# Kernel tuning notes

Measured on AMD Instinct MI355X. Metric: run time of the kernel, lower is better.

The kernel has to match this reference:

```python
import jax, jax.numpy as jnp
import numpy as np

EPS = 1e-5

def _proj(x, w, b, gamma, beta, mean, var):
    # 1x1 conv (einsum over channels) + BatchNorm (inference) ; Dropout is identity in eval.
    y = jnp.einsum('bchw,oc->bohw', x, w) + b[None, :, None, None]
    scale = gamma * jax.lax.rsqrt(var + EPS)
    shift = beta - mean * scale
    return y * scale[None, :, None, None] + shift[None, :, None, None]

def _make_layer(key, cin, cout):
    k1, k2, k3, k4 = jax.random.split(key, 4)
    w = jax.random.normal(k1, (cout, cin), jnp.float32) * (1.0 / np.sqrt(cin))
    b = jax.random.normal(k2, (cout,), jnp.float32) * 0.01
    gamma = 1.0 + 0.1 * jax.random.normal(k3, (cout,), jnp.float32)
    beta = 0.1 * jax.random.normal(k4, (cout,), jnp.float32)
    mean = 0.05 * jax.random.normal(jax.random.fold_in(k1, 7), (cout,), jnp.float32)
    var = 0.5 + jax.random.uniform(jax.random.fold_in(k2, 7), (cout,), jnp.float32)
    return w, b, gamma, beta, mean, var

def setup_inputs() -> dict:
    key = jax.random.key(0)
    B, C, Ci, H, W = 4, 128, 64, 64, 64
    ks = jax.random.split(key, 6)
    inp = {
        'x1': jax.random.normal(ks[0], (B, C, H, W), jnp.float32),
        'x2': jax.random.normal(ks[1], (B, C, H, W), jnp.float32),
    }
    for name, k, cin, cout in [('theta', ks[2], C, Ci), ('phi', ks[3], C, Ci),
                               ('g', ks[4], C, Ci), ('wout', ks[5], Ci, C)]:
        w, b, gm, bt, mn, vr = _make_layer(k, cin, cout)
        inp.update({f'{name}_w': w, f'{name}_b': b, f'{name}_g': gm,
                    f'{name}_beta': bt, f'{name}_m': mn, f'{name}_v': vr})
    return inp

def reference(x1, x2,
              theta_w, theta_b, theta_g, theta_beta, theta_m, theta_v,
              phi_w, phi_b, phi_g, phi_beta, phi_m, phi_v,
              g_w, g_b, g_g, g_beta, g_m, g_v,
              wout_w, wout_b, wout_g, wout_beta, wout_m, wout_v):
    B, C, H, W = x1.shape
    N = H * W
    theta_x1 = _proj(x1, theta_w, theta_b, theta_g, theta_beta, theta_m, theta_v).reshape(B, -1, N)  # [B,Ci,N]
    phi_x2 = _proj(x2, phi_w, phi_b, phi_g, phi_beta, phi_m, phi_v).reshape(B, -1, N)                # [B,Ci,N]
    g_x2 = _proj(x2, g_w, g_b, g_g, g_beta, g_m, g_v).reshape(B, -1, N)                              # [B,Ci,N]
    # attention_map[b, n, m] = sum_c theta[b,c,n] * phi[b,c,m]
    attn = jax.nn.softmax(jnp.einsum('bcn,bcm->bnm', theta_x1, phi_x2), axis=-1)  # [B,N,N]
    out = jnp.einsum('bnm,bcm->bcn', attn, g_x2).reshape(B, -1, H, W)             # [B,Ci,H,W]
    out = _proj(out, wout_w, wout_b, wout_g, wout_beta, wout_m, wout_v)           # [B,C,H,W]
    return jnp.concatenate((out, x1), axis=1)                                     # [B,2C,H,W]
```

## Files before the change

### kernel.cpp

```cpp
#include <hip/hip_runtime.h>
#include <stdint.h>
#include <stddef.h>

#define EPS   1e-5f
#define NB    4
#define CINCH 128
#define CI    64
#define NPIX  4096

typedef __bf16 bf16_t;
typedef bf16_t bf16x8 __attribute__((ext_vector_type(8)));
typedef float  f32x4  __attribute__((ext_vector_type(4)));

__device__ __forceinline__ f32x4 mfma16(bf16x8 a, bf16x8 b, f32x4 c) {
  return __builtin_amdgcn_mfma_f32_16x16x32_bf16(a, b, c, 0, 0, 0);
}
__device__ __forceinline__ f32x4 fzero4() {
  f32x4 z = {0.f, 0.f, 0.f, 0.f};
  return z;
}


__global__ __launch_bounds__(256) void proj_theta(
    const float* __restrict__ x1,
    const float* __restrict__ w,  const float* __restrict__ bb,
    const float* __restrict__ gm, const float* __restrict__ bt,
    const float* __restrict__ mn, const float* __restrict__ vr,
    bf16_t* __restrict__ thetaT_h, bf16_t* __restrict__ thetaT_l,
    float* __restrict__ out)
{
  __shared__ float wT[CINCH][CI];
  __shared__ float bfold[CI];
  const int tid = threadIdx.x;
  const int b   = blockIdx.y;
  const int n0  = blockIdx.x * 64;

  for (int idx = tid; idx < CI * CINCH; idx += 256) {
    const int o = idx & 63;
    const int c = idx >> 6;
    const float sc = gm[o] * rsqrtf(vr[o] + EPS);
    wT[c][o] = w[o * CINCH + c] * sc;
    if (c == 0) bfold[o] = bb[o] * sc + bt[o] - mn[o] * sc;
  }
  __syncthreads();

  const int n4 = tid & 15;
  const int og = tid >> 4;
  const float* xb = x1 + (size_t)b * CINCH * NPIX + n0 + n4 * 4;

  float acc[4][4];
#pragma unroll
  for (int j = 0; j < 4; ++j)
#pragma unroll
    for (int i = 0; i < 4; ++i) acc[j][i] = 0.f;

  for (int c0 = 0; c0 < CINCH; c0 += 4) {
    f32x4 xv[4];
#pragma unroll
    for (int cc = 0; cc < 4; ++cc)
      xv[cc] = *(const f32x4*)(xb + (size_t)(c0 + cc) * NPIX);
#pragma unroll
    for (int cc = 0; cc < 4; ++cc) {
      const f32x4 wv = *(const f32x4*)&wT[c0 + cc][og * 4];
#pragma unroll
      for (int j = 0; j < 4; ++j)
#pragma unroll
        for (int i = 0; i < 4; ++i)
          acc[j][i] += wv[j] * xv[cc][i];
    }
  }

#pragma unroll
  for (int j = 0; j < 4; ++j) {
    const int o = og * 4 + j;
    const float bias = bfold[o];
#pragma unroll
    for (int i = 0; i < 4; ++i) {
      const int n = n0 + n4 * 4 + i;
      const float v = acc[j][i] + bias;
      const bf16_t h = (bf16_t)v;
      const bf16_t l = (bf16_t)(v - (float)h);
      const size_t base = ((size_t)b * NPIX + n) * CI + o;
      thetaT_h[base] = h;
      thetaT_l[base] = l;
    }
  }

  for (int k = tid; k < CINCH * 64; k += 256) {
    const int c = k >> 6, nl = k & 63;
    out[((size_t)b * 256 + 128 + c) * NPIX + n0 + nl] =
        x1[((size_t)b * CINCH + c) * NPIX + n0 + nl];
  }
}

__global__ __launch_bounds__(256) void proj_phig(
    const float* __restrict__ x2,
    const float* __restrict__ pw,  const float* __restrict__ pb,
    const float* __restrict__ pg,  const float* __restrict__ pbt,
    const float* __restrict__ pm,  const float* __restrict__ pv,
    const float* __restrict__ gw,  const float* __restrict__ gb,
    const float* __restrict__ gg,  const float* __restrict__ gbt,
    const float* __restrict__ gmn, const float* __restrict__ gv,
    bf16_t* __restrict__ phiT_h, bf16_t* __restrict__ phiT_l,
    bf16_t* __restrict__ g_cm)
{
  __shared__ float wT[CINCH][128];
  __shared__ float bfold[128];
  const int tid = threadIdx.x;
  const int b   = blockIdx.y;
  const int n0  = blockIdx.x * 64;

  for (int idx = tid; idx < 128 * CINCH; idx += 256) {
    const int o  = idx & 127;
    const int c  = idx >> 7;
    const int oo = o & 63;
    float sc, wv_, bb_, bt_, mn_;
    if (o < 64) { sc = pg[oo] * rsqrtf(pv[oo] + EPS); wv_ = pw[oo*CINCH+c]; bb_ = pb[oo]; bt_ = pbt[oo]; mn_ = pm[oo]; }
    else        { sc = gg[oo] * rsqrtf(gv[oo] + EPS); wv_ = gw[oo*CINCH+c]; bb_ = gb[oo]; bt_ = gbt[oo]; mn_ = gmn[oo]; }
    wT[c][o] = wv_ * sc;
    if (c == 0) bfold[o] = bb_ * sc + bt_ - mn_ * sc;
  }
  __syncthreads();

  const int n4 = tid & 15;
  const int og = tid >> 4;
  const float* xb = x2 + (size_t)b * CINCH * NPIX + n0 + n4 * 4;

  float acc[8][4];
#pragma unroll
  for (int j = 0; j < 8; ++j)
#pragma unroll
    for (int i = 0; i < 4; ++i) acc[j][i] = 0.f;

  for (int c0 = 0; c0 < CINCH; c0 += 4) {
    f32x4 xv[4];
#pragma unroll
    for (int cc = 0; cc < 4; ++cc)
      xv[cc] = *(const f32x4*)(xb + (size_t)(c0 + cc) * NPIX);
#pragma unroll
    for (int cc = 0; cc < 4; ++cc) {
      const f32x4 wv0 = *(const f32x4*)&wT[c0 + cc][og * 8];
      const f32x4 wv1 = *(const f32x4*)&wT[c0 + cc][og * 8 + 4];
#pragma unroll
      for (int j = 0; j < 4; ++j)
#pragma unroll
        for (int i = 0; i < 4; ++i) {
          acc[j][i]     += wv0[j] * xv[cc][i];
          acc[j + 4][i] += wv1[j] * xv[cc][i];
        }
    }
  }

#pragma unroll
  for (int j = 0; j < 8; ++j) {
    const int o = og * 8 + j;
    const float bias = bfold[o];
#pragma unroll
    for (int i = 0; i < 4; ++i) {
      const int n = n0 + n4 * 4 + i;
      const float v = acc[j][i] + bias;
      if (o < 64) {
        const bf16_t h = (bf16_t)v;
        const bf16_t l = (bf16_t)(v - (float)h);
        const size_t rowb = ((size_t)b * NPIX + n) * 128;
        const int byte = (o * 2) ^ ((n & 7) << 4);
        *(bf16_t*)((char*)phiT_h + rowb + byte) = h;
        *(bf16_t*)((char*)phiT_l + rowb + byte) = l;
      } else {
        const int c = o - 64;
        const size_t base = ((size_t)b * CI + c) * (NPIX * 2);
        const int byte = ((n & ~63) * 2) + (((n & 63) * 2) ^ ((c & 7) << 4));
        *(bf16_t*)((char*)g_cm + base + byte) = (bf16_t)v;
      }
    }
  }
}

__global__ __launch_bounds__(256, 2) void flash_attn(
    const bf16_t* __restrict__ thetaT_h, const bf16_t* __restrict__ thetaT_l,
    const bf16_t* __restrict__ phiT_h,   const bf16_t* __restrict__ phiT_l,
    const bf16_t* __restrict__ g_cm,
    float* __restrict__ Opart, float* __restrict__ mlbuf)
{
  __shared__ __attribute__((aligned(16))) char sPhiH[64 * 128];
  __shared__ __attribute__((aligned(16))) char sPhiL[64 * 128];
  __shared__ __attribute__((aligned(16))) char sV[64 * 128];
  __shared__ __attribute__((aligned(16))) char sP[4][32 * 144];

  const int tid  = threadIdx.x;
  const int lane = tid & 63;
  const int wid  = tid >> 6;
  const int lrow = lane & 15;
  const int lhi  = lane >> 4;

  const int wg = blockIdx.x;
  const int b  = wg >> 7;
  const int qt = (wg & 127) >> 2;
  const int ks = wg & 3;
  const int q0 = qt * 128 + wid * 32;
  const int m0 = ks * 1024;

  bf16x8 qh[2][2], qlv[2][2];
  {
    const bf16_t* qbh = thetaT_h + ((size_t)b * NPIX + q0 + lrow) * CI + lhi * 8;
    const bf16_t* qbl = thetaT_l + ((size_t)b * NPIX + q0 + lrow) * CI + lhi * 8;
#pragma unroll
    for (int nt = 0; nt < 2; ++nt)
#pragma unroll
      for (int kk = 0; kk < 2; ++kk) {
        qh[nt][kk]  = *(const bf16x8*)(qbh + nt * 16 * CI + kk * 32);
        qlv[nt][kk] = *(const bf16x8*)(qbl + nt * 16 * CI + kk * 32);
      }
  }

  f32x4 oacc[2][4];
#pragma unroll
  for (int a = 0; a < 2; ++a)
#pragma unroll
    for (int c = 0; c < 4; ++c) oacc[a][c] = fzero4();

  float m_run[2] = {-1e30f, -1e30f};
  float l_run[2] = {0.f, 0.f};

  char* const Pw = sP[wid];

  for (int kb = 0; kb < 16; ++kb) {
    const int mg = m0 + kb * 64;
    __syncthreads();
    {
      const char* srcPH = (const char*)phiT_h + ((size_t)b * NPIX + mg) * 128;
      const char* srcPL = (const char*)phiT_l + ((size_t)b * NPIX + mg) * 128;
#pragma unroll
      for (int r = 0; r < 6; ++r) {
        const int chunk = r * 256 + tid;
        if (chunk < 512) {
          *(f32x4*)(sPhiH + chunk * 16) = *(const f32x4*)(srcPH + chunk * 16);
        } else if (chunk < 1024) {
          const int c2 = chunk - 512;
          *(f32x4*)(sPhiL + c2 * 16) = *(const f32x4*)(srcPL + c2 * 16);
        } else {
          const int c2  = chunk - 1024;
          const int row = c2 >> 3;
          const int col = (c2 & 7) * 16;
          *(f32x4*)(sV + row * 128 + col) =
              *(const f32x4*)((const char*)g_cm +
                              ((size_t)b * CI + row) * (NPIX * 2) + mg * 2 + col);
        }
      }
    }
    __syncthreads();

    f32x4 s[4][2];
#pragma unroll
    for (int mt = 0; mt < 4; ++mt)
#pragma unroll
      for (int nt = 0; nt < 2; ++nt) s[mt][nt] = fzero4();

#pragma unroll
    for (int mt = 0; mt < 4; ++mt) {
      const int row = mt * 16 + lrow;
      const int swz = (row & 7) << 4;
#pragma unroll
      for (int kk = 0; kk < 2; ++kk) {
        const int byte = row * 128 + ((kk * 64 + lhi * 16) ^ swz);
        const bf16x8 aH = *(const bf16x8*)(sPhiH + byte);
        const bf16x8 aL = *(const bf16x8*)(sPhiL + byte);
#pragma unroll
        for (int nt = 0; nt < 2; ++nt) {
          s[mt][nt] = mfma16(aH, qh[nt][kk],  s[mt][nt]);
          s[mt][nt] = mfma16(aH, qlv[nt][kk], s[mt][nt]);
          s[mt][nt] = mfma16(aL, qh[nt][kk],  s[mt][nt]);
        }
      }
    }

    float a2[2];
#pragma unroll
    for (int nt = 0; nt < 2; ++nt) {
      float mx = -1e30f;
#pragma unroll
      for (int mt = 0; mt < 4; ++mt)
#pragma unroll
        for (int r = 0; r < 4; ++r) mx = fmaxf(mx, s[mt][nt][r]);
      mx = fmaxf(mx, __shfl_xor(mx, 16));
      mx = fmaxf(mx, __shfl_xor(mx, 32));
      const float mnew  = fmaxf(m_run[nt], mx);
      const float alpha = __expf(m_run[nt] - mnew);
      float lsum = 0.f;
#pragma unroll
      for (int mt = 0; mt < 4; ++mt)
#pragma unroll
        for (int r = 0; r < 4; ++r) {
          const float p = __expf(s[mt][nt][r] - mnew);
          s[mt][nt][r] = p;
          lsum += p;
        }
      lsum += __shfl_xor(lsum, 16);
      lsum += __shfl_xor(lsum, 32);
      l_run[nt] = l_run[nt] * alpha + lsum;
      m_run[nt] = mnew;
      a2[nt] = alpha;
    }

#pragma unroll
    for (int qt2 = 0; qt2 < 2; ++qt2) {
#pragma unroll
      for (int r = 0; r < 4; ++r) {
        const float av = __shfl(a2[qt2], lhi * 4 + r);
#pragma unroll
        for (int ct = 0; ct < 4; ++ct) oacc[qt2][ct][r] *= av;
      }
    }

#pragma unroll
    for (int mt = 0; mt < 4; ++mt)
#pragma unroll
      for (int nt = 0; nt < 2; ++nt) {
        union { bf16_t h[4]; uint32_t u[2]; } pk;
#pragma unroll
        for (int r = 0; r < 4; ++r) pk.h[r] = (bf16_t)s[mt][nt][r];
        const int q    = nt * 16 + lrow;
        const int mloc = mt * 16 + lhi * 4;
        *(uint2*)(Pw + q * 144 + mloc * 2) = make_uint2(pk.u[0], pk.u[1]);
      }

    bf16x8 bV[2][4];
#pragma unroll
    for (int ct = 0; ct < 4; ++ct) {
      const int row = ct * 16 + lrow;
      const int swz = (row & 7) << 4;
#pragma unroll
      for (int kk = 0; kk < 2; ++kk)
        bV[kk][ct] = *(const bf16x8*)(sV + row * 128 + ((kk * 64 + lhi * 16) ^ swz));
    }
#pragma unroll
    for (int qt2 = 0; qt2 < 2; ++qt2) {
#pragma unroll
      for (int kk = 0; kk < 2; ++kk) {
        const bf16x8 pfrag =
            *(const bf16x8*)(Pw + (qt2 * 16 + lrow) * 144 + kk * 64 + lhi * 16);
#pragma unroll
        for (int ct = 0; ct < 4; ++ct)
          oacc[qt2][ct] = mfma16(pfrag, bV[kk][ct], oacc[qt2][ct]);
      }
    }
  }

#pragma unroll
  for (int qt2 = 0; qt2 < 2; ++qt2)
#pragma unroll
    for (int ct = 0; ct < 4; ++ct)
#pragma unroll
      for (int r = 0; r < 4; ++r) {
        const int q = q0 + qt2 * 16 + lhi * 4 + r;
        const int c = ct * 16 + lrow;
        Opart[(((size_t)b * NPIX + q) * 4 + ks) * 64 + c] = oacc[qt2][ct][r];
      }
  if (lhi < 2) {
    const int q = q0 + lhi * 16 + lrow;
    const size_t base = (((size_t)b * NPIX + q) * 4 + ks) * 2;
    mlbuf[base]     = m_run[lhi];
    mlbuf[base + 1] = l_run[lhi];
  }
}

__global__ __launch_bounds__(256) void merge_out(
    const float* __restrict__ Opart, const float* __restrict__ mlbuf,
    const float* __restrict__ ww,  const float* __restrict__ wb,
    const float* __restrict__ wg,  const float* __restrict__ wbt,
    const float* __restrict__ wm,  const float* __restrict__ wvv,
    float* __restrict__ out)
{
  __shared__ float wlds[128][64];
  __shared__ float bfold[128];
  const int tid = threadIdx.x;
  const int b   = blockIdx.y;
  const int n0  = blockIdx.x * 64;

  for (int idx = tid; idx < 128 * 64; idx += 256) {
    const int o = idx >> 6, c = idx & 63;
    const float sc = wg[o] * rsqrtf(wvv[o] + EPS);
    wlds[o][c] = ww[o * 64 + c] * sc;
    if (c == 0) bfold[o] = wb[o] * sc + wbt[o] - wm[o] * sc;
  }
  __syncthreads();

  const int ql = tid & 63;
  const int oh = tid >> 6;
  const int q  = n0 + ql;
  const size_t sb = ((size_t)b * NPIX + q) * 4;

  float mk[4], lk[4];
#pragma unroll
  for (int ks = 0; ks < 4; ++ks) {
    mk[ks] = mlbuf[(sb + ks) * 2];
    lk[ks] = mlbuf[(sb + ks) * 2 + 1];
  }
  const float M = fmaxf(fmaxf(mk[0], mk[1]), fmaxf(mk[2], mk[3]));
  float al[4]; float den = 0.f;
#pragma unroll
  for (int ks = 0; ks < 4; ++ks) { al[ks] = __expf(mk[ks] - M); den += al[ks] * lk[ks]; }
  const float inv = 1.f / den;
#pragma unroll
  for (int ks = 0; ks < 4; ++ks) al[ks] *= inv;

  float acc[32];
#pragma unroll
  for (int j = 0; j < 32; ++j) acc[j] = 0.f;

  for (int c0 = 0; c0 < 64; c0 += 4) {
    f32x4 mrg = {0.f, 0.f, 0.f, 0.f};
#pragma unroll
    for (int ks = 0; ks < 4; ++ks) {
      const f32x4 pv4 = *(const f32x4*)(Opart + (sb + ks) * 64 + c0);
      mrg += pv4 * al[ks];
    }
#pragma unroll
    for (int j = 0; j < 32; ++j) {
      const f32x4 wv4 = *(const f32x4*)&wlds[oh * 32 + j][c0];
      acc[j] += wv4[0] * mrg[0] + wv4[1] * mrg[1] + wv4[2] * mrg[2] + wv4[3] * mrg[3];
    }
  }

#pragma unroll
  for (int j = 0; j < 32; ++j) {
    const int o = oh * 32 + j;
    out[((size_t)b * 256 + o) * NPIX + q] = acc[j] + bfold[o];
  }
}

extern "C" void kernel_launch(void* const* d_in, const int* in_sizes, int n_in,
                              void* d_out, int out_size, void* d_ws, size_t ws_size,
                              hipStream_t stream) {
  (void)in_sizes; (void)n_in; (void)out_size; (void)ws_size;
  const float* x1  = (const float*)d_in[0];
  const float* x2  = (const float*)d_in[1];
  const float* tw  = (const float*)d_in[2];
  const float* tb  = (const float*)d_in[3];
  const float* tg  = (const float*)d_in[4];
  const float* tbt = (const float*)d_in[5];
  const float* tm  = (const float*)d_in[6];
  const float* tv  = (const float*)d_in[7];
  const float* pw  = (const float*)d_in[8];
  const float* pb  = (const float*)d_in[9];
  const float* pg  = (const float*)d_in[10];
  const float* pbt = (const float*)d_in[11];
  const float* pm  = (const float*)d_in[12];
  const float* pv  = (const float*)d_in[13];
  const float* gw  = (const float*)d_in[14];
  const float* gb  = (const float*)d_in[15];
  const float* gg  = (const float*)d_in[16];
  const float* gbt = (const float*)d_in[17];
  const float* gmn = (const float*)d_in[18];
  const float* gv  = (const float*)d_in[19];
  const float* ww  = (const float*)d_in[20];
  const float* wb  = (const float*)d_in[21];
  const float* wg  = (const float*)d_in[22];
  const float* wbt = (const float*)d_in[23];
  const float* wm  = (const float*)d_in[24];
  const float* wv  = (const float*)d_in[25];

  float* out = (float*)d_out;
  char*  ws  = (char*)d_ws;
  bf16_t* thetaT_h = (bf16_t*)(ws);
  bf16_t* thetaT_l = (bf16_t*)(ws + (size_t)(2)  * 1048576);
  bf16_t* phiT_h   = (bf16_t*)(ws + (size_t)(4)  * 1048576);
  bf16_t* phiT_l   = (bf16_t*)(ws + (size_t)(6)  * 1048576);
  bf16_t* g_cm     = (bf16_t*)(ws + (size_t)(8)  * 1048576);
  float*  Opart    = (float*) (ws + (size_t)(10) * 1048576);
  float*  mlbuf    = (float*) (ws + (size_t)(26) * 1048576);

  dim3 gp(64, 4);
  proj_theta<<<gp, 256, 0, stream>>>(x1, tw, tb, tg, tbt, tm, tv,
                                     thetaT_h, thetaT_l, out);
  proj_phig<<<gp, 256, 0, stream>>>(x2, pw, pb, pg, pbt, pm, pv,
                                    gw, gb, gg, gbt, gmn, gv,
                                    phiT_h, phiT_l, g_cm);
  flash_attn<<<512, 256, 0, stream>>>(thetaT_h, thetaT_l, phiT_h, phiT_l,
                                      g_cm, Opart, mlbuf);
  merge_out<<<gp, 256, 0, stream>>>(Opart, mlbuf, ww, wb, wg, wbt, wm, wv, out);
}
```

Measured before the change: 260.6 us.

## Double-buffer attention tiles via async global-to-LDS loads and retile projection kernels

The flash attention loop now stages phi and g tiles into a double-buffered LDS region using global_load_lds, so loading the next key block overlaps compute on the current one and one barrier per iteration is dropped. The projection kernels are split (phi and g into separate kernels) and switched to 32-pixel tiles with an LDS transpose, so outputs go out as vectorized 16-byte bf16 stores instead of scalar ones. The merge kernel is restructured to merge partials into LDS first, then run the output projection with twice as many blocks. The extra kernel launch, the added LDS use, and the more complex ordering around the async loads are the costs.

```diff
diff --git a/kernel.cpp b/kernel.cpp
--- a/kernel.cpp
+++ b/kernel.cpp
@@ -3,7 +3,6 @@
 #include <stddef.h>
 
 #define EPS   1e-5f
-#define NB    4
 #define CINCH 128
 #define CI    64
 #define NPIX  4096
@@ -12,12 +11,18 @@
 typedef bf16_t bf16x8 __attribute__((ext_vector_type(8)));
 typedef float  f32x4  __attribute__((ext_vector_type(4)));
 
+typedef __attribute__((address_space(3))) unsigned int lds_u32;
+typedef __attribute__((address_space(1))) const unsigned int glb_u32;
+
 __device__ __forceinline__ f32x4 mfma16(bf16x8 a, bf16x8 b, f32x4 c) {
   return __builtin_amdgcn_mfma_f32_16x16x32_bf16(a, b, c, 0, 0, 0);
 }
 __device__ __forceinline__ f32x4 fzero4() {
   f32x4 z = {0.f, 0.f, 0.f, 0.f};
   return z;
+}
+__device__ __forceinline__ void gload16(const void* g, void* l) {
+  __builtin_amdgcn_global_load_lds((glb_u32*)g, (lds_u32*)l, 16, 0, 0);
 }
 
 
@@ -31,148 +36,202 @@
 {
   __shared__ float wT[CINCH][CI];
   __shared__ float bfold[CI];
+  __shared__ float tileF[32][68];
+
   const int tid = threadIdx.x;
   const int b   = blockIdx.y;
-  const int n0  = blockIdx.x * 64;
+  const int n0  = blockIdx.x * 32;
 
   for (int idx = tid; idx < CI * CINCH; idx += 256) {
-    const int o = idx & 63;
-    const int c = idx >> 6;
+    const int o = idx & 63, c = idx >> 6;
     const float sc = gm[o] * rsqrtf(vr[o] + EPS);
     wT[c][o] = w[o * CINCH + c] * sc;
     if (c == 0) bfold[o] = bb[o] * sc + bt[o] - mn[o] * sc;
   }
   __syncthreads();
 
-  const int n4 = tid & 15;
-  const int og = tid >> 4;
-  const float* xb = x1 + (size_t)b * CINCH * NPIX + n0 + n4 * 4;
-
-  float acc[4][4];
-#pragma unroll
-  for (int j = 0; j < 4; ++j)
-#pragma unroll
-    for (int i = 0; i < 4; ++i) acc[j][i] = 0.f;
-
+  const int px = tid & 31;
+  const int og = tid >> 5;
+  const float* xb = x1 + (size_t)b * CINCH * NPIX + n0 + px;
+
+  float acc[8];
+#pragma unroll
+  for (int j = 0; j < 8; ++j) acc[j] = 0.f;
+
+#pragma unroll 4
   for (int c0 = 0; c0 < CINCH; c0 += 4) {
-    f32x4 xv[4];
-#pragma unroll
-    for (int cc = 0; cc < 4; ++cc)
-      xv[cc] = *(const f32x4*)(xb + (size_t)(c0 + cc) * NPIX);
+    float xv[4];
+#pragma unroll
+    for (int cc = 0; cc < 4; ++cc) xv[cc] = xb[(size_t)(c0 + cc) * NPIX];
 #pragma unroll
     for (int cc = 0; cc < 4; ++cc) {
-      const f32x4 wv = *(const f32x4*)&wT[c0 + cc][og * 4];
-#pragma unroll
-      for (int j = 0; j < 4; ++j)
-#pragma unroll
-        for (int i = 0; i < 4; ++i)
-          acc[j][i] += wv[j] * xv[cc][i];
-    }
-  }
-
-#pragma unroll
-  for (int j = 0; j < 4; ++j) {
-    const int o = og * 4 + j;
-    const float bias = bfold[o];
-#pragma unroll
-    for (int i = 0; i < 4; ++i) {
-      const int n = n0 + n4 * 4 + i;
-      const float v = acc[j][i] + bias;
+      const f32x4 w0 = *(const f32x4*)&wT[c0 + cc][og * 8];
+      const f32x4 w1 = *(const f32x4*)&wT[c0 + cc][og * 8 + 4];
+#pragma unroll
+      for (int j = 0; j < 4; ++j) {
+        acc[j]     += w0[j] * xv[cc];
+        acc[j + 4] += w1[j] * xv[cc];
+      }
+    }
+  }
+#pragma unroll
+  for (int j = 0; j < 8; ++j) tileF[px][og * 8 + j] = acc[j] + bfold[og * 8 + j];
+  __syncthreads();
+
+  {
+    const int px2 = tid >> 3, ogs = tid & 7;
+    bf16x8 hv, lv;
+#pragma unroll
+    for (int j = 0; j < 8; ++j) {
+      const float v = tileF[px2][ogs * 8 + j];
       const bf16_t h = (bf16_t)v;
-      const bf16_t l = (bf16_t)(v - (float)h);
-      const size_t base = ((size_t)b * NPIX + n) * CI + o;
-      thetaT_h[base] = h;
-      thetaT_l[base] = l;
-    }
-  }
-
-  for (int k = tid; k < CINCH * 64; k += 256) {
-    const int c = k >> 6, nl = k & 63;
-    out[((size_t)b * 256 + 128 + c) * NPIX + n0 + nl] =
-        x1[((size_t)b * CINCH + c) * NPIX + n0 + nl];
-  }
-}
-
-__global__ __launch_bounds__(256) void proj_phig(
+      hv[j] = h;
+      lv[j] = (bf16_t)(v - (float)h);
+    }
+    const size_t base = ((size_t)b * NPIX + n0 + px2) * CI + ogs * 8;
+    *(bf16x8*)(thetaT_h + base) = hv;
+    *(bf16x8*)(thetaT_l + base) = lv;
+  }
+
+#pragma unroll
+  for (int i = 0; i < 4; ++i) {
+    const int idx = i * 256 + tid;
+    const int c = idx >> 3, n4 = (idx & 7) * 4;
+    *(f32x4*)(out + ((size_t)b * 256 + 128 + c) * NPIX + n0 + n4) =
+        *(const f32x4*)(x1 + ((size_t)b * CINCH + c) * NPIX + n0 + n4);
+  }
+}
+
+__global__ __launch_bounds__(256) void proj_phi(
     const float* __restrict__ x2,
-    const float* __restrict__ pw,  const float* __restrict__ pb,
-    const float* __restrict__ pg,  const float* __restrict__ pbt,
-    const float* __restrict__ pm,  const float* __restrict__ pv,
-    const float* __restrict__ gw,  const float* __restrict__ gb,
-    const float* __restrict__ gg,  const float* __restrict__ gbt,
-    const float* __restrict__ gmn, const float* __restrict__ gv,
-    bf16_t* __restrict__ phiT_h, bf16_t* __restrict__ phiT_l,
+    const float* __restrict__ w,  const float* __restrict__ bb,
+    const float* __restrict__ gm, const float* __restrict__ bt,
+    const float* __restrict__ mn, const float* __restrict__ vr,
+    bf16_t* __restrict__ phiT_h, bf16_t* __restrict__ phiT_l)
+{
+  __shared__ float wT[CINCH][CI];
+  __shared__ float bfold[CI];
+  __shared__ float tileF[32][68];
+
+  const int tid = threadIdx.x;
+  const int b   = blockIdx.y;
+  const int n0  = blockIdx.x * 32;
+
+  for (int idx = tid; idx < CI * CINCH; idx += 256) {
+    const int o = idx & 63, c = idx >> 6;
+    const float sc = gm[o] * rsqrtf(vr[o] + EPS);
+    wT[c][o] = w[o * CINCH + c] * sc;
+    if (c == 0) bfold[o] = bb[o] * sc + bt[o] - mn[o] * sc;
+  }
+  __syncthreads();
+
+  const int px = tid & 31;
+  const int og = tid >> 5;
+  const float* xb = x2 + (size_t)b * CINCH * NPIX + n0 + px;
+
+  float acc[8];
+#pragma unroll
+  for (int j = 0; j < 8; ++j) acc[j] = 0.f;
+
+#pragma unroll 4
+  for (int c0 = 0; c0 < CINCH; c0 += 4) {
+    float xv[4];
+#pragma unroll
+    for (int cc = 0; cc < 4; ++cc) xv[cc] = xb[(size_t)(c0 + cc) * NPIX];
+#pragma unroll
+    for (int cc = 0; cc < 4; ++cc) {
+      const f32x4 w0 = *(const f32x4*)&wT[c0 + cc][og * 8];
+      const f32x4 w1 = *(const f32x4*)&wT[c0 + cc][og * 8 + 4];
+#pragma unroll
+      for (int j = 0; j < 4; ++j) {
+        acc[j]     += w0[j] * xv[cc];
+        acc[j + 4] += w1[j] * xv[cc];
+      }
+    }
+  }
+#pragma unroll
+  for (int j = 0; j < 8; ++j) tileF[px][og * 8 + j] = acc[j] + bfold[og * 8 + j];
+  __syncthreads();
+
+  {
+    const int px2 = tid >> 3, ogs = tid & 7;
+    const int n = n0 + px2;
+    bf16x8 hv, lv;
+#pragma unroll
+    for (int j = 0; j < 8; ++j) {
+      const float v = tileF[px2][ogs * 8 + j];
+      const bf16_t h = (bf16_t)v;
+      hv[j] = h;
+      lv[j] = (bf16_t)(v - (float)h);
+    }
+    const size_t rowb = ((size_t)b * NPIX + n) * 128;
+    const int byte = (ogs * 16) ^ ((n & 7) << 4);
+    *(bf16x8*)((char*)phiT_h + rowb + byte) = hv;
+    *(bf16x8*)((char*)phiT_l + rowb + byte) = lv;
+  }
+}
+
+__global__ __launch_bounds__(256) void proj_g(
+    const float* __restrict__ x2,
+    const float* __restrict__ w,  const float* __restrict__ bb,
+    const float* __restrict__ gm, const float* __restrict__ bt,
+    const float* __restrict__ mn, const float* __restrict__ vr,
     bf16_t* __restrict__ g_cm)
 {
-  __shared__ float wT[CINCH][128];
-  __shared__ float bfold[128];
+  __shared__ float wT[CINCH][CI];
+  __shared__ float bfold[CI];
+  __shared__ float gT[CI][33];
+
   const int tid = threadIdx.x;
   const int b   = blockIdx.y;
-  const int n0  = blockIdx.x * 64;
-
-  for (int idx = tid; idx < 128 * CINCH; idx += 256) {
-    const int o  = idx & 127;
-    const int c  = idx >> 7;
-    const int oo = o & 63;
-    float sc, wv_, bb_, bt_, mn_;
-    if (o < 64) { sc = pg[oo] * rsqrtf(pv[oo] + EPS); wv_ = pw[oo*CINCH+c]; bb_ = pb[oo]; bt_ = pbt[oo]; mn_ = pm[oo]; }
-    else        { sc = gg[oo] * rsqrtf(gv[oo] + EPS); wv_ = gw[oo*CINCH+c]; bb_ = gb[oo]; bt_ = gbt[oo]; mn_ = gmn[oo]; }
-    wT[c][o] = wv_ * sc;
-    if (c == 0) bfold[o] = bb_ * sc + bt_ - mn_ * sc;
-  }
-  __syncthreads();
-
-  const int n4 = tid & 15;
-  const int og = tid >> 4;
-  const float* xb = x2 + (size_t)b * CINCH * NPIX + n0 + n4 * 4;
-
-  float acc[8][4];
-#pragma unroll
-  for (int j = 0; j < 8; ++j)
-#pragma unroll
-    for (int i = 0; i < 4; ++i) acc[j][i] = 0.f;
-
+  const int n0  = blockIdx.x * 32;
+
+  for (int idx = tid; idx < CI * CINCH; idx += 256) {
+    const int o = idx & 63, c = idx >> 6;
+    const float sc = gm[o] * rsqrtf(vr[o] + EPS);
+    wT[c][o] = w[o * CINCH + c] * sc;
+    if (c == 0) bfold[o] = bb[o] * sc + bt[o] - mn[o] * sc;
+  }
+  __syncthreads();
+
+  const int px = tid & 31;
+  const int og = tid >> 5;
+  const float* xb = x2 + (size_t)b * CINCH * NPIX + n0 + px;
+
+  float acc[8];
+#pragma unroll
+  for (int j = 0; j < 8; ++j) acc[j] = 0.f;
+
+#pragma unroll 4
   for (int c0 = 0; c0 < CINCH; c0 += 4) {
-    f32x4 xv[4];
-#pragma unroll
-    for (int cc = 0; cc < 4; ++cc)
-      xv[cc] = *(const f32x4*)(xb + (size_t)(c0 + cc) * NPIX);
+    float xv[4];
+#pragma unroll
+    for (int cc = 0; cc < 4; ++cc) xv[cc] = xb[(size_t)(c0 + cc) * NPIX];
 #pragma unroll
     for (int cc = 0; cc < 4; ++cc) {
-      const f32x4 wv0 = *(const f32x4*)&wT[c0 + cc][og * 8];
-      const f32x4 wv1 = *(const f32x4*)&wT[c0 + cc][og * 8 + 4];
-#pragma unroll
-      for (int j = 0; j < 4; ++j)
-#pragma unroll
-        for (int i = 0; i < 4; ++i) {
-          acc[j][i]     += wv0[j] * xv[cc][i];
-          acc[j + 4][i] += wv1[j] * xv[cc][i];
-        }
-    }
-  }
-
-#pragma unroll
-  for (int j = 0; j < 8; ++j) {
-    const int o = og * 8 + j;
-    const float bias = bfold[o];
-#pragma unroll
-    for (int i = 0; i < 4; ++i) {
-      const int n = n0 + n4 * 4 + i;
-      const float v = acc[j][i] + bias;
-      if (o < 64) {
-        const bf16_t h = (bf16_t)v;
-        const bf16_t l = (bf16_t)(v - (float)h);
-        const size_t rowb = ((size_t)b * NPIX + n) * 128;
-        const int byte = (o * 2) ^ ((n & 7) << 4);
-        *(bf16_t*)((char*)phiT_h + rowb + byte) = h;
-        *(bf16_t*)((char*)phiT_l + rowb + byte) = l;
-      } else {
-        const int c = o - 64;
-        const size_t base = ((size_t)b * CI + c) * (NPIX * 2);
-        const int byte = ((n & ~63) * 2) + (((n & 63) * 2) ^ ((c & 7) << 4));
-        *(bf16_t*)((char*)g_cm + base + byte) = (bf16_t)v;
-      }
-    }
+      const f32x4 w0 = *(const f32x4*)&wT[c0 + cc][og * 8];
+      const f32x4 w1 = *(const f32x4*)&wT[c0 + cc][og * 8 + 4];
+#pragma unroll
+      for (int j = 0; j < 4; ++j) {
+        acc[j]     += w0[j] * xv[cc];
+        acc[j + 4] += w1[j] * xv[cc];
+      }
+    }
+  }
+#pragma unroll
+  for (int j = 0; j < 8; ++j) gT[og * 8 + j][px] = acc[j] + bfold[og * 8 + j];
+  __syncthreads();
+
+  {
+    const int c  = tid & 63;
+    const int mgp = tid >> 6;
+    bf16x8 gv;
+#pragma unroll
+    for (int j = 0; j < 8; ++j) gv[j] = (bf16_t)gT[c][mgp * 8 + j];
+    const int m = n0 + mgp * 8;
+    char* rowc = (char*)g_cm + ((size_t)b * CI + c) * (NPIX * 2);
+    const int byte = ((m & ~63) * 2) + ((((m & 63) * 2) ^ ((c & 7) << 4)));
+    *(bf16x8*)(rowc + byte) = gv;
   }
 }
 
@@ -182,9 +241,7 @@
     const bf16_t* __restrict__ g_cm,
     float* __restrict__ Opart, float* __restrict__ mlbuf)
 {
-  __shared__ __attribute__((aligned(16))) char sPhiH[64 * 128];
-  __shared__ __attribute__((aligned(16))) char sPhiL[64 * 128];
-  __shared__ __attribute__((aligned(16))) char sV[64 * 128];
+  __shared__ __attribute__((aligned(16))) char sTile[2][24576];
   __shared__ __attribute__((aligned(16))) char sP[4][32 * 144];
 
   const int tid  = threadIdx.x;
@@ -200,6 +257,27 @@
   const int q0 = qt * 128 + wid * 32;
   const int m0 = ks * 1024;
 
+  const char* const srcPHb = (const char*)phiT_h + ((size_t)b * NPIX) * 128;
+  const char* const srcPLb = (const char*)phiT_l + ((size_t)b * NPIX) * 128;
+  const char* const srcVb  = (const char*)g_cm + (size_t)b * CI * (NPIX * 2);
+
+  auto stage = [&](int buf, int kb) {
+    const int mg = m0 + kb * 64;
+    const char* srcPH = srcPHb + (size_t)mg * 128;
+    const char* srcPL = srcPLb + (size_t)mg * 128;
+    const char* srcV  = srcVb + (size_t)mg * 2;
+    char* const dst = sTile[buf];
+    int c;
+    c = tid;       gload16(srcPH + c * 16, dst + c * 16);
+    c = 256 + tid; gload16(srcPH + c * 16, dst + c * 16);
+    c = tid;       gload16(srcPL + c * 16, dst + 8192 + c * 16);
+    c = 256 + tid; gload16(srcPL + c * 16, dst + 8192 + c * 16);
+    c = tid;       gload16(srcV + (size_t)(c >> 3) * (NPIX * 2) + (c & 7) * 16,
+                           dst + 16384 + c * 16);
+    c = 256 + tid; gload16(srcV + (size_t)(c >> 3) * (NPIX * 2) + (c & 7) * 16,
+                           dst + 16384 + c * 16);
+  };
+
   bf16x8 qh[2][2], qlv[2][2];
   {
     const bf16_t* qbh = thetaT_h + ((size_t)b * NPIX + q0 + lrow) * CI + lhi * 8;
@@ -224,31 +302,16 @@
 
   char* const Pw = sP[wid];
 
+  stage(0, 0);
+  __syncthreads();
+
   for (int kb = 0; kb < 16; ++kb) {
-    const int mg = m0 + kb * 64;
-    __syncthreads();
-    {
-      const char* srcPH = (const char*)phiT_h + ((size_t)b * NPIX + mg) * 128;
-      const char* srcPL = (const char*)phiT_l + ((size_t)b * NPIX + mg) * 128;
-#pragma unroll
-      for (int r = 0; r < 6; ++r) {
-        const int chunk = r * 256 + tid;
-        if (chunk < 512) {
-          *(f32x4*)(sPhiH + chunk * 16) = *(const f32x4*)(srcPH + chunk * 16);
-        } else if (chunk < 1024) {
-          const int c2 = chunk - 512;
-          *(f32x4*)(sPhiL + c2 * 16) = *(const f32x4*)(srcPL + c2 * 16);
-        } else {
-          const int c2  = chunk - 1024;
-          const int row = c2 >> 3;
-          const int col = (c2 & 7) * 16;
-          *(f32x4*)(sV + row * 128 + col) =
-              *(const f32x4*)((const char*)g_cm +
-                              ((size_t)b * CI + row) * (NPIX * 2) + mg * 2 + col);
-        }
-      }
-    }
-    __syncthreads();
+    const int cur = kb & 1;
+    if (kb < 15) stage(cur ^ 1, kb + 1);
+
+    const char* const sPhiH = sTile[cur];
+    const char* const sPhiL = sTile[cur] + 8192;
+    const char* const sV    = sTile[cur] + 16384;
 
     f32x4 s[4][2];
 #pragma unroll
@@ -344,6 +407,8 @@
           oacc[qt2][ct] = mfma16(pfrag, bV[kk][ct], oacc[qt2][ct]);
       }
     }
+
+    if (kb < 15) __syncthreads();
   }
 
 #pragma unroll
@@ -372,60 +437,71 @@
     float* __restrict__ out)
 {
   __shared__ float wlds[128][64];
-  __shared__ float bfold[128];
+  __shared__ float bfw[128];
+  __shared__ float mrg[32][68];
+
   const int tid = threadIdx.x;
   const int b   = blockIdx.y;
-  const int n0  = blockIdx.x * 64;
+  const int n0  = blockIdx.x * 32;
 
   for (int idx = tid; idx < 128 * 64; idx += 256) {
     const int o = idx >> 6, c = idx & 63;
     const float sc = wg[o] * rsqrtf(wvv[o] + EPS);
     wlds[o][c] = ww[o * 64 + c] * sc;
-    if (c == 0) bfold[o] = wb[o] * sc + wbt[o] - wm[o] * sc;
-  }
-  __syncthreads();
-
-  const int ql = tid & 63;
-  const int oh = tid >> 6;
-  const int q  = n0 + ql;
-  const size_t sb = ((size_t)b * NPIX + q) * 4;
-
-  float mk[4], lk[4];
-#pragma unroll
-  for (int ks = 0; ks < 4; ++ks) {
-    mk[ks] = mlbuf[(sb + ks) * 2];
-    lk[ks] = mlbuf[(sb + ks) * 2 + 1];
-  }
-  const float M = fmaxf(fmaxf(mk[0], mk[1]), fmaxf(mk[2], mk[3]));
-  float al[4]; float den = 0.f;
-#pragma unroll
-  for (int ks = 0; ks < 4; ++ks) { al[ks] = __expf(mk[ks] - M); den += al[ks] * lk[ks]; }
-  const float inv = 1.f / den;
-#pragma unroll
-  for (int ks = 0; ks < 4; ++ks) al[ks] *= inv;
-
-  float acc[32];
-#pragma unroll
-  for (int j = 0; j < 32; ++j) acc[j] = 0.f;
-
+    if (c == 0) bfw[o] = wb[o] * sc + wbt[o] - wm[o] * sc;
+  }
+
+  {
+    const int px = tid & 31;
+    const int cg = tid >> 5;
+    const int q  = n0 + px;
+    const size_t sb = ((size_t)b * NPIX + q) * 4;
+    float mk[4], lk[4];
+#pragma unroll
+    for (int ks = 0; ks < 4; ++ks) {
+      mk[ks] = mlbuf[(sb + ks) * 2];
+      lk[ks] = mlbuf[(sb + ks) * 2 + 1];
+    }
+    const float M = fmaxf(fmaxf(mk[0], mk[1]), fmaxf(mk[2], mk[3]));
+    float al[4]; float den = 0.f;
+#pragma unroll
+    for (int ks = 0; ks < 4; ++ks) { al[ks] = __expf(mk[ks] - M); den += al[ks] * lk[ks]; }
+    const float inv = 1.f / den;
+#pragma unroll
+    for (int ks = 0; ks < 4; ++ks) al[ks] *= inv;
+
+    f32x4 r0 = fzero4(), r1 = fzero4();
+#pragma unroll
+    for (int ks = 0; ks < 4; ++ks) {
+      const f32x4 p0 = *(const f32x4*)(Opart + (sb + ks) * 64 + cg * 8);
+      const f32x4 p1 = *(const f32x4*)(Opart + (sb + ks) * 64 + cg * 8 + 4);
+      r0 += p0 * al[ks];
+      r1 += p1 * al[ks];
+    }
+    *(f32x4*)&mrg[px][cg * 8]     = r0;
+    *(f32x4*)&mrg[px][cg * 8 + 4] = r1;
+  }
+  __syncthreads();
+
+  const int px = tid & 31;
+  const int oh = tid >> 5;
+  float acc[16];
+#pragma unroll
+  for (int j = 0; j < 16; ++j) acc[j] = 0.f;
+
+#pragma unroll 4
   for (int c0 = 0; c0 < 64; c0 += 4) {
-    f32x4 mrg = {0.f, 0.f, 0.f, 0.f};
-#pragma unroll
-    for (int ks = 0; ks < 4; ++ks) {
-      const f32x4 pv4 = *(const f32x4*)(Opart + (sb + ks) * 64 + c0);
-      mrg += pv4 * al[ks];
-    }
-#pragma unroll
-    for (int j = 0; j < 32; ++j) {
-      const f32x4 wv4 = *(const f32x4*)&wlds[oh * 32 + j][c0];
-      acc[j] += wv4[0] * mrg[0] + wv4[1] * mrg[1] + wv4[2] * mrg[2] + wv4[3] * mrg[3];
-    }
-  }
-
-#pragma unroll
-  for (int j = 0; j < 32; ++j) {
-    const int o = oh * 32 + j;
-    out[((size_t)b * 256 + o) * NPIX + q] = acc[j] + bfold[o];
+    const f32x4 m4 = *(const f32x4*)&mrg[px][c0];
+#pragma unroll
+    for (int j = 0; j < 16; ++j) {
+      const f32x4 w4 = *(const f32x4*)&wlds[oh * 16 + j][c0];
+      acc[j] += w4[0] * m4[0] + w4[1] * m4[1] + w4[2] * m4[2] + w4[3] * m4[3];
+    }
+  }
+#pragma unroll
+  for (int j = 0; j < 16; ++j) {
+    const int o = oh * 16 + j;
+    out[((size_t)b * 256 + o) * NPIX + n0 + px] = acc[j] + bfw[o];
   }
 }
 
@@ -470,12 +546,12 @@
   float*  Opart    = (float*) (ws + (size_t)(10) * 1048576);
   float*  mlbuf    = (float*) (ws + (size_t)(26) * 1048576);
 
-  dim3 gp(64, 4);
+  dim3 gp(128, 4);
   proj_theta<<<gp, 256, 0, stream>>>(x1, tw, tb, tg, tbt, tm, tv,
                                      thetaT_h, thetaT_l, out);
-  proj_phig<<<gp, 256, 0, stream>>>(x2, pw, pb, pg, pbt, pm, pv,
-                                    gw, gb, gg, gbt, gmn, gv,
-                                    phiT_h, phiT_l, g_cm);
+  proj_phi<<<gp, 256, 0, stream>>>(x2, pw, pb, pg, pbt, pm, pv,
+                                   phiT_h, phiT_l);
+  proj_g<<<gp, 256, 0, stream>>>(x2, gw, gb, gg, gbt, gmn, gv, g_cm);
   flash_attn<<<512, 256, 0, stream>>>(thetaT_h, thetaT_l, phiT_h, phiT_l,
                                       g_cm, Opart, mlbuf);
   merge_out<<<gp, 256, 0, stream>>>(Opart, mlbuf, ww, wb, wg, wbt, wm, wv, out);
```

Measured after the change: 238.3 us. 8.6% less time.
